# Kernel tuning notes

Measured on AMD Instinct MI355X. Metric: run time of the kernel, lower is better.

## Reference

```python
import jax, jax.numpy as jnp
import numpy as np

B, S, D, H = 1, 2048, 768, 12
E, K, I = 8, 2, 1024          # routed experts, top-k, expert inter dim
IS = 2 * I                    # shared-expert inter dim (n_shared_experts * moe_inter_dim)
EPS = 1e-5
ROUTE_SCALE = 1.0


def rmsnorm(x, w, eps=EPS):
    xf = x.astype(jnp.float32)
    return (xf * jax.lax.rsqrt(jnp.mean(xf * xf, axis=-1, keepdims=True) + eps)).astype(x.dtype) * w


def setup_inputs() -> dict:
    key = jax.random.key(0)
    ks = jax.random.split(key, 8)
    sc = 0.02
    return {
        "x": jax.random.normal(ks[0], (B, S, D), jnp.float32),
        "norm1_w": jnp.ones((D,), jnp.float32),
        "norm3_w": jnp.ones((D,), jnp.float32),
        "gate_w": jax.random.normal(ks[1], (E, D), jnp.float32) * sc,
        "w1": jax.random.normal(ks[2], (E, I, D), jnp.float32) * sc,
        "b1": jnp.zeros((E, I), jnp.float32),
        "w2": jax.random.normal(ks[3], (E, D, I), jnp.float32) * sc,
        "b2": jnp.zeros((E, D), jnp.float32),
        "w3": jax.random.normal(ks[4], (E, I, D), jnp.float32) * sc,
        "b3": jnp.zeros((E, I), jnp.float32),
        "fc1_w": jax.random.normal(ks[5], (IS, D), jnp.float32) * sc,
        "fc1_b": jnp.zeros((IS,), jnp.float32),
        "fc2_w": jax.random.normal(ks[6], (D, IS), jnp.float32) * sc,
        "fc2_b": jnp.zeros((D,), jnp.float32),
    }


def _forward(x, norm1_w, norm3_w, gate_w, w1, b1, w2, b2, w3, b3,
             fc1_w, fc1_b, fc2_w, fc2_b):
    b, s, d = x.shape
    hd = d // H

    # ---- self-attention (no qkv/out projections in the original module) ----
    xn = rmsnorm(x, norm1_w)
    qkv = xn.reshape(b, s, H, hd).transpose(0, 2, 1, 3)      # [b,h,s,hd]
    scores = jnp.einsum("bhqd,bhkd->bhqk", qkv, qkv) / np.sqrt(hd)
    attn = jax.nn.softmax(scores, axis=-1)
    ao = jnp.einsum("bhqk,bhkd->bhqd", attn, qkv)
    attn_out = ao.transpose(0, 2, 1, 3).reshape(b, s, d)
    out = x + attn_out

    # ---- MoE on norm3(out) ----
    xf = rmsnorm(out, norm3_w).reshape(-1, d)                # [N, D]
    n = xf.shape[0]

    # Gate: softmax scoring, n_groups=1 (no group masking), no bias (dim != 7168)
    logits = xf @ gate_w.T                                    # [N, E]
    sc = jax.nn.softmax(logits.astype(jnp.float32), axis=-1)  # max-subtract folded in
    _, idx = jax.lax.top_k(sc, K)                             # [N, K]
    weights = jnp.take_along_axis(sc, idx, axis=-1)
    weights = jnp.clip(weights, 1e-7) * ROUTE_SCALE
    weights = weights.astype(xf.dtype)

    # combine matrix: per-token dense expert weights (zeros for unselected)
    cmb = jnp.zeros((n, E), xf.dtype).at[jnp.arange(n)[:, None], idx].add(weights)

    # SwiGLU experts, batched over E (zero combine weight == not dispatched)
    a = jnp.einsum("nd,eid->nei", xf, w1) + b1                # [N,E,I]
    g = jnp.einsum("nd,eid->nei", xf, w3) + b3
    h = jax.nn.silu(a) * g
    eo = jnp.einsum("nei,edi->ned", h, w2) + b2               # [N,E,D]
    y = jnp.einsum("ned,ne->nd", eo, cmb)

    # shared experts (SiLU MLP)
    z = jax.nn.silu(xf @ fc1_w.T + fc1_b) @ fc2_w.T + fc2_b

    moe_out = (y + z).reshape(b, s, d)
    return out + moe_out


def reference(x, norm1_w, norm3_w, gate_w, w1, b1, w2, b2, w3, b3,
              fc1_w, fc1_b, fc2_w, fc2_b):
    return _forward(x, norm1_w, norm3_w, gate_w, w1, b1, w2, b2, w3, b3,
                    fc1_w, fc1_b, fc2_w, fc2_b)
```

## Files before the change

### kernel.cpp

```cpp
#include <hip/hip_runtime.h>
#include <math.h>

#define SEQ    2048
#define DMODEL 768
#define NHEAD  12
#define NEXP   8
#define IDIM   1024
#define ISH    2048
#define KVS    4
#define NE2    10

typedef unsigned short u16;
typedef short s16x8 __attribute__((ext_vector_type(8)));
typedef u16   u16x8 __attribute__((ext_vector_type(8)));
typedef float f32x4 __attribute__((ext_vector_type(4)));

#define MFMA_BF16(a, b, c) __builtin_amdgcn_mfma_f32_16x16x32_bf16((a), (b), (c), 0, 0, 0)

__device__ __forceinline__ void glds16(const void* g, void* l) {
  __builtin_amdgcn_global_load_lds(
      (const __attribute__((address_space(1))) unsigned int*)g,
      (__attribute__((address_space(3))) unsigned int*)l, 16, 0, 0);
}

__device__ __forceinline__ u16 f2b(float f) {
  unsigned int u = __float_as_uint(f);
  unsigned int r = u + 0x7fffu + ((u >> 16) & 1u);
  return (u16)(r >> 16);
}
__device__ __forceinline__ float b2f(u16 v) {
  return __uint_as_float(((unsigned int)v) << 16);
}

#define CVT_BLOCKS 10752

__global__ __launch_bounds__(256) void prep_kernel(
    const float* __restrict__ w1, const float* __restrict__ w3, const float* __restrict__ w2,
    const float* __restrict__ fc1, const float* __restrict__ fc2,
    u16* __restrict__ w1b, u16* __restrict__ w3b, u16* __restrict__ w2b,
    u16* __restrict__ fc1b, u16* __restrict__ fc2b, int* __restrict__ counts,
    const float* __restrict__ x, const float* __restrict__ norm1_w, u16* __restrict__ xnb) {
  __shared__ float red[256];
  const int tid = threadIdx.x;
  if (blockIdx.x < CVT_BLOCKS) {
    if (blockIdx.x == 0 && tid < 16) counts[tid] = 0;
    long i = (long)blockIdx.x * 256 + tid;
    const long NW8 = (long)NEXP * IDIM * DMODEL / 8;
    const long NF8 = (long)ISH * DMODEL / 8;
    const float* s; u16* d; long o;
    if      (i < NW8)             { s = w1;  d = w1b;  o = i; }
    else if (i < 2 * NW8)         { s = w3;  d = w3b;  o = i - NW8; }
    else if (i < 3 * NW8)         { s = w2;  d = w2b;  o = i - 2 * NW8; }
    else if (i < 3 * NW8 + NF8)   { s = fc1; d = fc1b; o = i - 3 * NW8; }
    else                          { s = fc2; d = fc2b; o = i - 3 * NW8 - NF8; }
    float4 a = ((const float4*)s)[2 * o], b = ((const float4*)s)[2 * o + 1];
    u16x8 v;
    v[0] = f2b(a.x); v[1] = f2b(a.y); v[2] = f2b(a.z); v[3] = f2b(a.w);
    v[4] = f2b(b.x); v[5] = f2b(b.y); v[6] = f2b(b.z); v[7] = f2b(b.w);
    ((u16x8*)d)[o] = v;
    return;
  }
  const int row = blockIdx.x - CVT_BLOCKS;
  const float* r = x + (size_t)row * DMODEL;
  float v0 = r[tid], v1 = r[tid + 256], v2 = r[tid + 512];
  float ss = v0 * v0 + v1 * v1 + v2 * v2;
  red[tid] = ss;
  __syncthreads();
  for (int s = 128; s > 0; s >>= 1) {
    if (tid < s) red[tid] += red[tid + s];
    __syncthreads();
  }
  float rms = rsqrtf(red[0] * (1.f / DMODEL) + 1e-5f);
  u16* ob = xnb + (size_t)row * DMODEL;
  ob[tid]       = f2b(v0 * rms * norm1_w[tid]);
  ob[tid + 256] = f2b(v1 * rms * norm1_w[tid + 256]);
  ob[tid + 512] = f2b(v2 * rms * norm1_w[tid + 512]);
}

__global__ __launch_bounds__(256) void attn_kernel(const u16* __restrict__ xnb,
                                                   u16* __restrict__ Opart,
                                                   float* __restrict__ Mpart,
                                                   float* __restrict__ Lpart) {
  __shared__ u16 Qs[64][72];
  __shared__ u16 Ks[64][72];
  __shared__ u16 Vt[64][72];
  __shared__ u16 Ps[64][72];
  const int h = blockIdx.y, kvs = blockIdx.z;
  const int q0 = blockIdx.x * 64;
  const int tid = threadIdx.x;
  const int lane = tid & 63, w = tid >> 6;
  const int quad = lane >> 4, l15 = lane & 15;
  const size_t hoff = (size_t)h * 64;

  for (int cc = tid; cc < 512; cc += 256) {
    int row = cc >> 3, col8 = (cc & 7) * 8;
    *(u16x8*)&Qs[row][col8] = *(const u16x8*)(xnb + (size_t)(q0 + row) * DMODEL + hoff + col8);
  }
  __syncthreads();
  const s16x8 aq0 = *(const s16x8*)&Qs[16 * w + l15][quad * 8];
  const s16x8 aq1 = *(const s16x8*)&Qs[16 * w + l15][32 + quad * 8];

  f32x4 o[4] = {};
  float mrow[4], lrow[4];
#pragma unroll
  for (int r = 0; r < 4; r++) { mrow[r] = -INFINITY; lrow[r] = 0.f; }

  const int it0 = kvs * (SEQ / 64 / KVS);
  for (int it = 0; it < SEQ / 64 / KVS; it++) {
    const int k0 = (it0 + it) * 64;
    for (int cc = tid; cc < 512; cc += 256) {
      int row = cc >> 3, col8 = (cc & 7) * 8;
      *(u16x8*)&Ks[row][col8] = *(const u16x8*)(xnb + (size_t)(k0 + row) * DMODEL + hoff + col8);
    }
    __syncthreads();

    {
      const int rp = tid & 31, dc = ((tid >> 5) & 7) * 8;
      u16x8 v0 = *(const u16x8*)&Ks[2 * rp][dc];
      u16x8 v1 = *(const u16x8*)&Ks[2 * rp + 1][dc];
#pragma unroll
      for (int j = 0; j < 8; j++) {
        *(unsigned int*)&Vt[dc + j][2 * rp] =
            (unsigned int)v0[j] | ((unsigned int)v1[j] << 16);
      }
    }

    f32x4 s4[4] = {};
#pragma unroll
    for (int jt = 0; jt < 4; jt++) {
      s16x8 b0 = *(const s16x8*)&Ks[16 * jt + l15][quad * 8];
      s16x8 b1 = *(const s16x8*)&Ks[16 * jt + l15][32 + quad * 8];
      s4[jt] = MFMA_BF16(aq0, b0, s4[jt]);
      s4[jt] = MFMA_BF16(aq1, b1, s4[jt]);
      s4[jt] *= 0.125f;
    }

#pragma unroll
    for (int r = 0; r < 4; r++) {
      float mx = mrow[r];
#pragma unroll
      for (int jt = 0; jt < 4; jt++) mx = fmaxf(mx, s4[jt][r]);
#pragma unroll
      for (int m = 1; m <= 8; m <<= 1) mx = fmaxf(mx, __shfl_xor(mx, m, 64));
      float al = __expf(mrow[r] - mx);
      mrow[r] = mx;
      float pv[4], sum = 0.f;
#pragma unroll
      for (int jt = 0; jt < 4; jt++) { pv[jt] = __expf(s4[jt][r] - mx); sum += pv[jt]; }
#pragma unroll
      for (int m = 1; m <= 8; m <<= 1) sum += __shfl_xor(sum, m, 64);
      lrow[r] = lrow[r] * al + sum;
#pragma unroll
      for (int jt = 0; jt < 4; jt++) o[jt][r] *= al;
#pragma unroll
      for (int jt = 0; jt < 4; jt++) Ps[16 * w + quad * 4 + r][16 * jt + l15] = f2b(pv[jt]);
    }
    __syncthreads();

    s16x8 ap0 = *(const s16x8*)&Ps[16 * w + l15][quad * 8];
    s16x8 ap1 = *(const s16x8*)&Ps[16 * w + l15][32 + quad * 8];
#pragma unroll
    for (int jt = 0; jt < 4; jt++) {
      s16x8 bv0 = *(const s16x8*)&Vt[16 * jt + l15][quad * 8];
      s16x8 bv1 = *(const s16x8*)&Vt[16 * jt + l15][32 + quad * 8];
      o[jt] = MFMA_BF16(ap0, bv0, o[jt]);
      o[jt] = MFMA_BF16(ap1, bv1, o[jt]);
    }
  }

  const size_t base = ((size_t)kvs * NHEAD + h) * SEQ;
#pragma unroll
  for (int r = 0; r < 4; r++) {
    int q = q0 + 16 * w + quad * 4 + r;
#pragma unroll
    for (int jt = 0; jt < 4; jt++)
      Opart[(base + q) * 64 + 16 * jt + l15] = f2b(o[jt][r]);
    if (l15 == 0) {
      Mpart[base + q] = mrow[r];
      Lpart[base + q] = lrow[r];
    }
  }
}

__global__ __launch_bounds__(256) void fused_post_kernel(
    const u16* __restrict__ Opart, const float* __restrict__ Mpart,
    const float* __restrict__ Lpart, const float* __restrict__ x,
    const float* __restrict__ n3w, const float* __restrict__ gw,
    u16* __restrict__ xfb, float* __restrict__ out,
    int* __restrict__ counts, int* __restrict__ toklist, float* __restrict__ wtlist) {
  const int t = blockIdx.x;
  const int tid = threadIdx.x;
  __shared__ float Ms[KVS * NHEAD], Ls[KVS * NHEAD];
  __shared__ float red[256];
  __shared__ float gred[4][NEXP];
  if (tid < KVS * NHEAD) {
    Ms[tid] = Mpart[(size_t)tid * SEQ + t];
    Ls[tid] = Lpart[(size_t)tid * SEQ + t];
  }
  __syncthreads();

  float val[3];
  float ss = 0.f;
#pragma unroll
  for (int ii = 0; ii < 3; ii++) {
    int c = tid + ii * 256;
    int h = c >> 6, d = c & 63;
    float M = -INFINITY;
#pragma unroll
    for (int k = 0; k < KVS; k++) M = fmaxf(M, Ms[k * NHEAD + h]);
    float L = 0.f, O = 0.f;
#pragma unroll
    for (int k = 0; k < KVS; k++) {
      float wgt = __expf(Ms[k * NHEAD + h] - M);
      L += wgt * Ls[k * NHEAD + h];
      O += wgt * b2f(Opart[((size_t)(k * NHEAD + h) * SEQ + t) * 64 + d]);
    }
    float v = x[(size_t)t * DMODEL + c] + O / L;
    out[(size_t)t * DMODEL + c] = v;
    val[ii] = v;
    ss += v * v;
  }
  red[tid] = ss;
  __syncthreads();
  for (int s = 128; s > 0; s >>= 1) {
    if (tid < s) red[tid] += red[tid + s];
    __syncthreads();
  }
  float rms = rsqrtf(red[0] * (1.f / DMODEL) + 1e-5f);

  float ge[NEXP] = {};
#pragma unroll
  for (int ii = 0; ii < 3; ii++) {
    int c = tid + ii * 256;
    float xn = val[ii] * rms * n3w[c];
    xfb[(size_t)t * DMODEL + c] = f2b(xn);
#pragma unroll
    for (int e = 0; e < NEXP; e++) ge[e] = fmaf(xn, gw[e * DMODEL + c], ge[e]);
  }
  const int lane = tid & 63, w = tid >> 6;
#pragma unroll
  for (int off = 32; off >= 1; off >>= 1)
#pragma unroll
    for (int e = 0; e < NEXP; e++) ge[e] += __shfl_xor(ge[e], off, 64);
  if (lane == 0)
#pragma unroll
    for (int e = 0; e < NEXP; e++) gred[w][e] = ge[e];
  __syncthreads();
  if (tid == 0) {
    float p[NEXP], mx = -INFINITY, s = 0.f;
#pragma unroll
    for (int e = 0; e < NEXP; e++) {
      p[e] = gred[0][e] + gred[1][e] + gred[2][e] + gred[3][e];
      mx = fmaxf(mx, p[e]);
    }
#pragma unroll
    for (int e = 0; e < NEXP; e++) { p[e] = __expf(p[e] - mx); s += p[e]; }
    int e0 = 0; float b0 = p[0];
    for (int e = 1; e < NEXP; e++) if (p[e] > b0) { b0 = p[e]; e0 = e; }
    int e1 = -1; float b1v = -1.f;
    for (int e = 0; e < NEXP; e++) if (e != e0 && p[e] > b1v) { b1v = p[e]; e1 = e; }
    float inv = 1.f / s;
    int pos0 = atomicAdd(&counts[e0], 1);
    toklist[e0 * SEQ + pos0] = t;
    wtlist[e0 * SEQ + pos0] = fmaxf(b0 * inv, 1e-7f);
    int pos1 = atomicAdd(&counts[e1], 1);
    toklist[e1 * SEQ + pos1] = t;
    wtlist[e1 * SEQ + pos1] = fmaxf(b1v * inv, 1e-7f);
  }
}

__global__ __launch_bounds__(256) void gemm1_kernel(
    const u16* __restrict__ xfb,
    const u16* __restrict__ w1b, const u16* __restrict__ w3b, const u16* __restrict__ fc1b,
    const float* __restrict__ b1, const float* __restrict__ b3, const float* __restrict__ fc1_b,
    const int* __restrict__ counts, const int* __restrict__ toklist, u16* __restrict__ hb) {
  __shared__ u16 As0[64][32],  As1[64][32];
  __shared__ u16 W1s0[128][32], W1s1[128][32];
  __shared__ u16 W3s0[128][32], W3s1[128][32];
  __shared__ int rIdx[64];
  const int L = blockIdx.x;
  const int g = L & 7, s = L >> 3;
  const int T = g * 320 + s;
  const int e = T >> 8;
  const int rem = T & 255;
  const int mt = rem >> 3, nt = rem & 7;
  const bool routed = (e < NEXP);
  int cnt, off;
  if (routed) {
    cnt = counts[e];
    off = 0;
    for (int i = 0; i < e; i++) off += counts[i];
  } else {
    cnt = SEQ;
    off = 2 * SEQ + (e - NEXP) * SEQ;
  }
  const int m0 = mt * 64;
  if (m0 >= cnt) return;
  const int n0 = nt * 128;
  const int tid = threadIdx.x;
  if (tid < 64) {
    int rr = m0 + tid;
    rIdx[tid] = routed ? toklist[e * SEQ + (rr < cnt ? rr : cnt - 1)] : rr;
  }
  __syncthreads();
  const u16* W1 = routed ? w1b + (size_t)e * IDIM * DMODEL
                         : fc1b + (size_t)(e - NEXP) * IDIM * DMODEL;
  const u16* W3 = w3b + (size_t)(routed ? e : 0) * IDIM * DMODEL;

  const int lane = tid & 63, w = tid >> 6;
  const int quad = lane >> 4, l15 = lane & 15;
  const int wy = w >> 1, wx = w & 1;
  const int rsub = lane >> 2, c8 = (lane & 3) * 8;
  const u16* Ap   = xfb + (size_t)rIdx[16 * w + rsub] * DMODEL + c8;
  const u16* W1p0 = W1 + (size_t)(n0 + 32 * w + rsub) * DMODEL + c8;
  const u16* W1p1 = W1 + (size_t)(n0 + 32 * w + 16 + rsub) * DMODEL + c8;
  const u16* W3p0 = W3 + (size_t)(n0 + 32 * w + rsub) * DMODEL + c8;
  const u16* W3p1 = W3 + (size_t)(n0 + 32 * w + 16 + rsub) * DMODEL + c8;

  f32x4 acc1[2][4] = {};
  f32x4 acc3[2][4] = {};
  for (int k0 = 0; k0 < DMODEL; k0 += 64) {
    glds16(Ap + k0,        &As0[16 * w][0]);
    glds16(Ap + k0 + 32,   &As1[16 * w][0]);
    glds16(W1p0 + k0,      &W1s0[32 * w][0]);
    glds16(W1p1 + k0,      &W1s0[32 * w + 16][0]);
    glds16(W1p0 + k0 + 32, &W1s1[32 * w][0]);
    glds16(W1p1 + k0 + 32, &W1s1[32 * w + 16][0]);
    if (routed) {
      glds16(W3p0 + k0,      &W3s0[32 * w][0]);
      glds16(W3p1 + k0,      &W3s0[32 * w + 16][0]);
      glds16(W3p0 + k0 + 32, &W3s1[32 * w][0]);
      glds16(W3p1 + k0 + 32, &W3s1[32 * w + 16][0]);
    }
    __syncthreads();
    s16x8 af0[2], af1[2], w1f0[4], w1f1[4];
#pragma unroll
    for (int i = 0; i < 2; i++) {
      af0[i] = *(const s16x8*)&As0[32 * wy + 16 * i + l15][quad * 8];
      af1[i] = *(const s16x8*)&As1[32 * wy + 16 * i + l15][quad * 8];
    }
#pragma unroll
    for (int j = 0; j < 4; j++) {
      w1f0[j] = *(const s16x8*)&W1s0[64 * wx + 16 * j + l15][quad * 8];
      w1f1[j] = *(const s16x8*)&W1s1[64 * wx + 16 * j + l15][quad * 8];
    }
#pragma unroll
    for (int i = 0; i < 2; i++)
#pragma unroll
      for (int j = 0; j < 4; j++) {
        acc1[i][j] = MFMA_BF16(af0[i], w1f0[j], acc1[i][j]);
        acc1[i][j] = MFMA_BF16(af1[i], w1f1[j], acc1[i][j]);
      }
    if (routed) {
      s16x8 w3f0[4], w3f1[4];
#pragma unroll
      for (int j = 0; j < 4; j++) {
        w3f0[j] = *(const s16x8*)&W3s0[64 * wx + 16 * j + l15][quad * 8];
        w3f1[j] = *(const s16x8*)&W3s1[64 * wx + 16 * j + l15][quad * 8];
      }
#pragma unroll
      for (int i = 0; i < 2; i++)
#pragma unroll
        for (int j = 0; j < 4; j++) {
          acc3[i][j] = MFMA_BF16(af0[i], w3f0[j], acc3[i][j]);
          acc3[i][j] = MFMA_BF16(af1[i], w3f1[j], acc3[i][j]);
        }
    }
    __syncthreads();
  }

#pragma unroll
  for (int j = 0; j < 4; j++) {
    int n = n0 + 64 * wx + 16 * j + l15;
    float b1v = routed ? b1[e * IDIM + n] : fc1_b[(e - NEXP) * IDIM + n];
    float b3v = routed ? b3[e * IDIM + n] : 0.f;
#pragma unroll
    for (int i = 0; i < 2; i++) {
#pragma unroll
      for (int r = 0; r < 4; r++) {
        int rr = m0 + 32 * wy + 16 * i + quad * 4 + r;
        if (rr < cnt) {
          float a = acc1[i][j][r] + b1v;
          float gg = routed ? (acc3[i][j][r] + b3v) : 1.f;
          float hv = a / (1.f + __expf(-a)) * gg;
          hb[(size_t)(off + rr) * IDIM + n] = f2b(hv);
        }
      }
    }
  }
}

__global__ __launch_bounds__(256) void gemm2_kernel(
    const u16* __restrict__ hb,
    const u16* __restrict__ w2b, const u16* __restrict__ fc2b,
    const float* __restrict__ b2, const float* __restrict__ fc2_b,
    const int* __restrict__ counts, const int* __restrict__ toklist,
    const float* __restrict__ wtlist, float* __restrict__ out) {
  __shared__ u16 As0[64][32],  As1[64][32];
  __shared__ u16 Ws0[128][32], Ws1[128][32];
  const int L = blockIdx.x;
  const int g = L & 7, s = L >> 3;
  const int T = g * 240 + s;
  const int e = T / 192;
  const int rem = T - e * 192;
  const int mt = rem / 6, nt = rem - mt * 6;
  const bool routed = (e < NEXP);
  int cnt, off;
  if (routed) {
    cnt = counts[e];
    off = 0;
    for (int i = 0; i < e; i++) off += counts[i];
  } else {
    cnt = SEQ;
    off = 2 * SEQ + (e - NEXP) * SEQ;
  }
  const int m0 = mt * 64;
  if (m0 >= cnt) return;
  const int n0 = nt * 128;
  const int tid = threadIdx.x;

  const u16* Wb; int ldw, kof;
  if (routed) { Wb = w2b + (size_t)e * DMODEL * IDIM; ldw = IDIM; kof = 0; }
  else        { Wb = fc2b;                            ldw = ISH;  kof = (e - NEXP) * IDIM; }

  const int lane = tid & 63, w = tid >> 6;
  const int quad = lane >> 4, l15 = lane & 15;
  const int wy = w >> 1, wx = w & 1;
  const int rsub = lane >> 2, c8 = (lane & 3) * 8;
  int ra = m0 + 16 * w + rsub; ra = off + (ra < cnt ? ra : cnt - 1);
  const u16* Ap  = hb + (size_t)ra * IDIM + c8;
  const u16* Wp0 = Wb + (size_t)(n0 + 32 * w + rsub) * ldw + kof + c8;
  const u16* Wp1 = Wb + (size_t)(n0 + 32 * w + 16 + rsub) * ldw + kof + c8;

  f32x4 acc[2][4] = {};
  for (int k0 = 0; k0 < IDIM; k0 += 64) {
    glds16(Ap + k0,        &As0[16 * w][0]);
    glds16(Ap + k0 + 32,   &As1[16 * w][0]);
    glds16(Wp0 + k0,       &Ws0[32 * w][0]);
    glds16(Wp1 + k0,       &Ws0[32 * w + 16][0]);
    glds16(Wp0 + k0 + 32,  &Ws1[32 * w][0]);
    glds16(Wp1 + k0 + 32,  &Ws1[32 * w + 16][0]);
    __syncthreads();
    s16x8 af0[2], af1[2], wf0[4], wf1[4];
#pragma unroll
    for (int i = 0; i < 2; i++) {
      af0[i] = *(const s16x8*)&As0[32 * wy + 16 * i + l15][quad * 8];
      af1[i] = *(const s16x8*)&As1[32 * wy + 16 * i + l15][quad * 8];
    }
#pragma unroll
    for (int j = 0; j < 4; j++) {
      wf0[j] = *(const s16x8*)&Ws0[64 * wx + 16 * j + l15][quad * 8];
      wf1[j] = *(const s16x8*)&Ws1[64 * wx + 16 * j + l15][quad * 8];
    }
#pragma unroll
    for (int i = 0; i < 2; i++)
#pragma unroll
      for (int j = 0; j < 4; j++) {
        acc[i][j] = MFMA_BF16(af0[i], wf0[j], acc[i][j]);
        acc[i][j] = MFMA_BF16(af1[i], wf1[j], acc[i][j]);
      }
    __syncthreads();
  }

#pragma unroll
  for (int j = 0; j < 4; j++) {
    int n = n0 + 64 * wx + 16 * j + l15;
    float bv = routed ? b2[e * DMODEL + n] : (e == NEXP ? fc2_b[n] : 0.f);
#pragma unroll
    for (int i = 0; i < 2; i++) {
#pragma unroll
      for (int r = 0; r < 4; r++) {
        int rr = m0 + 32 * wy + 16 * i + quad * 4 + r;
        if (rr < cnt) {
          int tok; float wt;
          if (routed) { tok = toklist[e * SEQ + rr]; wt = wtlist[e * SEQ + rr]; }
          else        { tok = rr;                    wt = 1.f; }
          atomicAdd(&out[(size_t)tok * DMODEL + n], wt * (acc[i][j][r] + bv));
        }
      }
    }
  }
}

extern "C" void kernel_launch(void* const* d_in, const int* in_sizes, int n_in,
                              void* d_out, int out_size, void* d_ws, size_t ws_size,
                              hipStream_t stream) {
  const float* x       = (const float*)d_in[0];
  const float* norm1_w = (const float*)d_in[1];
  const float* norm3_w = (const float*)d_in[2];
  const float* gate_w  = (const float*)d_in[3];
  const float* w1      = (const float*)d_in[4];
  const float* b1      = (const float*)d_in[5];
  const float* w2      = (const float*)d_in[6];
  const float* b2      = (const float*)d_in[7];
  const float* w3      = (const float*)d_in[8];
  const float* b3      = (const float*)d_in[9];
  const float* fc1_w   = (const float*)d_in[10];
  const float* fc1_b   = (const float*)d_in[11];
  const float* fc2_w   = (const float*)d_in[12];
  const float* fc2_b   = (const float*)d_in[13];
  float* out = (float*)d_out;

  char* p = (char*)d_ws;
  u16*   xnb    = (u16*)p;   p += (size_t)SEQ * DMODEL * 2;
  u16*   xfb    = (u16*)p;   p += (size_t)SEQ * DMODEL * 2;
  u16*   hb     = (u16*)p;   p += (size_t)4 * SEQ * IDIM * 2;
  u16*   Opart  = (u16*)p;   p += (size_t)KVS * NHEAD * SEQ * 64 * 2;
  float* Mpart  = (float*)p; p += (size_t)KVS * NHEAD * SEQ * 4;
  float* Lpart  = (float*)p; p += (size_t)KVS * NHEAD * SEQ * 4;
  u16*   w1b    = (u16*)p;   p += (size_t)NEXP * IDIM * DMODEL * 2;
  u16*   w3b    = (u16*)p;   p += (size_t)NEXP * IDIM * DMODEL * 2;
  u16*   w2b    = (u16*)p;   p += (size_t)NEXP * DMODEL * IDIM * 2;
  u16*   fc1b   = (u16*)p;   p += (size_t)ISH * DMODEL * 2;
  u16*   fc2b   = (u16*)p;   p += (size_t)DMODEL * ISH * 2;
  int*   counts = (int*)p;   p += 256;
  int*   toklist= (int*)p;   p += (size_t)NEXP * SEQ * 4;
  float* wtlist = (float*)p; p += (size_t)NEXP * SEQ * 4;

  prep_kernel<<<CVT_BLOCKS + SEQ, 256, 0, stream>>>(
      w1, w3, w2, fc1_w, fc2_w, w1b, w3b, w2b, fc1b, fc2b, counts, x, norm1_w, xnb);
  attn_kernel<<<dim3(SEQ / 64, NHEAD, KVS), 256, 0, stream>>>(xnb, Opart, Mpart, Lpart);
  fused_post_kernel<<<SEQ, 256, 0, stream>>>(Opart, Mpart, Lpart, x, norm3_w, gate_w,
                                             xfb, out, counts, toklist, wtlist);
  gemm1_kernel<<<2560, 256, 0, stream>>>(
      xfb, w1b, w3b, fc1b, b1, b3, fc1_b, counts, toklist, hb);
  gemm2_kernel<<<1920, 256, 0, stream>>>(
      hb, w2b, fc2b, b2, fc2_b, counts, toklist, wtlist, out);
  (void)in_sizes; (void)n_in; (void)out_size; (void)ws_size;
}
```

Before: 376.4 us.

## Stream expert weights directly to registers and double-buffer activation tiles in LDS

```diff
diff --git a/kernel.cpp b/kernel.cpp
--- a/kernel.cpp
+++ b/kernel.cpp
@@ -274,9 +274,7 @@
     const u16* __restrict__ w1b, const u16* __restrict__ w3b, const u16* __restrict__ fc1b,
     const float* __restrict__ b1, const float* __restrict__ b3, const float* __restrict__ fc1_b,
     const int* __restrict__ counts, const int* __restrict__ toklist, u16* __restrict__ hb) {
-  __shared__ u16 As0[64][32],  As1[64][32];
-  __shared__ u16 W1s0[128][32], W1s1[128][32];
-  __shared__ u16 W3s0[128][32], W3s1[128][32];
+  __shared__ u16 Abuf[2][2][64][32];
   __shared__ int rIdx[64];
   const int L = blockIdx.x;
   const int g = L & 7, s = L >> 3;
@@ -311,62 +309,51 @@
   const int quad = lane >> 4, l15 = lane & 15;
   const int wy = w >> 1, wx = w & 1;
   const int rsub = lane >> 2, c8 = (lane & 3) * 8;
-  const u16* Ap   = xfb + (size_t)rIdx[16 * w + rsub] * DMODEL + c8;
-  const u16* W1p0 = W1 + (size_t)(n0 + 32 * w + rsub) * DMODEL + c8;
-  const u16* W1p1 = W1 + (size_t)(n0 + 32 * w + 16 + rsub) * DMODEL + c8;
-  const u16* W3p0 = W3 + (size_t)(n0 + 32 * w + rsub) * DMODEL + c8;
-  const u16* W3p1 = W3 + (size_t)(n0 + 32 * w + 16 + rsub) * DMODEL + c8;
+  const u16* Ap  = xfb + (size_t)rIdx[16 * w + rsub] * DMODEL + c8;
+  const u16* W1r = W1 + (size_t)(n0 + 64 * wx + l15) * DMODEL + quad * 8;
+  const u16* W3r = W3 + (size_t)(n0 + 64 * wx + l15) * DMODEL + quad * 8;
 
   f32x4 acc1[2][4] = {};
   f32x4 acc3[2][4] = {};
-  for (int k0 = 0; k0 < DMODEL; k0 += 64) {
-    glds16(Ap + k0,        &As0[16 * w][0]);
-    glds16(Ap + k0 + 32,   &As1[16 * w][0]);
-    glds16(W1p0 + k0,      &W1s0[32 * w][0]);
-    glds16(W1p1 + k0,      &W1s0[32 * w + 16][0]);
-    glds16(W1p0 + k0 + 32, &W1s1[32 * w][0]);
-    glds16(W1p1 + k0 + 32, &W1s1[32 * w + 16][0]);
-    if (routed) {
-      glds16(W3p0 + k0,      &W3s0[32 * w][0]);
-      glds16(W3p1 + k0,      &W3s0[32 * w + 16][0]);
-      glds16(W3p0 + k0 + 32, &W3s1[32 * w][0]);
-      glds16(W3p1 + k0 + 32, &W3s1[32 * w + 16][0]);
-    }
+  const int NK = DMODEL / 64;
+
+  glds16(Ap, &Abuf[0][0][16 * w][0]);
+  glds16(Ap + 32, &Abuf[0][1][16 * w][0]);
+
+  for (int kt = 0; kt < NK; kt++) {
     __syncthreads();
-    s16x8 af0[2], af1[2], w1f0[4], w1f1[4];
-#pragma unroll
-    for (int i = 0; i < 2; i++) {
-      af0[i] = *(const s16x8*)&As0[32 * wy + 16 * i + l15][quad * 8];
-      af1[i] = *(const s16x8*)&As1[32 * wy + 16 * i + l15][quad * 8];
-    }
-#pragma unroll
-    for (int j = 0; j < 4; j++) {
-      w1f0[j] = *(const s16x8*)&W1s0[64 * wx + 16 * j + l15][quad * 8];
-      w1f1[j] = *(const s16x8*)&W1s1[64 * wx + 16 * j + l15][quad * 8];
-    }
-#pragma unroll
-    for (int i = 0; i < 2; i++)
-#pragma unroll
-      for (int j = 0; j < 4; j++) {
-        acc1[i][j] = MFMA_BF16(af0[i], w1f0[j], acc1[i][j]);
-        acc1[i][j] = MFMA_BF16(af1[i], w1f1[j], acc1[i][j]);
+    const int b = kt & 1;
+    if (kt + 1 < NK) {
+      glds16(Ap + (kt + 1) * 64, &Abuf[b ^ 1][0][16 * w][0]);
+      glds16(Ap + (kt + 1) * 64 + 32, &Abuf[b ^ 1][1][16 * w][0]);
+    }
+#pragma unroll
+    for (int p = 0; p < 2; p++) {
+      const int kc = kt * 64 + 32 * p;
+      s16x8 af[2];
+      af[0] = *(const s16x8*)&Abuf[b][p][32 * wy + l15][quad * 8];
+      af[1] = *(const s16x8*)&Abuf[b][p][32 * wy + 16 + l15][quad * 8];
+      s16x8 w1f[4];
+#pragma unroll
+      for (int j = 0; j < 4; j++)
+        w1f[j] = *(const s16x8*)(W1r + (size_t)(16 * j) * DMODEL + kc);
+#pragma unroll
+      for (int i = 0; i < 2; i++)
+#pragma unroll
+        for (int j = 0; j < 4; j++)
+          acc1[i][j] = MFMA_BF16(af[i], w1f[j], acc1[i][j]);
+      if (routed) {
+        s16x8 w3f[4];
+#pragma unroll
+        for (int j = 0; j < 4; j++)
+          w3f[j] = *(const s16x8*)(W3r + (size_t)(16 * j) * DMODEL + kc);
+#pragma unroll
+        for (int i = 0; i < 2; i++)
+#pragma unroll
+          for (int j = 0; j < 4; j++)
+            acc3[i][j] = MFMA_BF16(af[i], w3f[j], acc3[i][j]);
       }
-    if (routed) {
-      s16x8 w3f0[4], w3f1[4];
-#pragma unroll
-      for (int j = 0; j < 4; j++) {
-        w3f0[j] = *(const s16x8*)&W3s0[64 * wx + 16 * j + l15][quad * 8];
-        w3f1[j] = *(const s16x8*)&W3s1[64 * wx + 16 * j + l15][quad * 8];
-      }
-#pragma unroll
-      for (int i = 0; i < 2; i++)
-#pragma unroll
-        for (int j = 0; j < 4; j++) {
-          acc3[i][j] = MFMA_BF16(af0[i], w3f0[j], acc3[i][j]);
-          acc3[i][j] = MFMA_BF16(af1[i], w3f1[j], acc3[i][j]);
-        }
-    }
-    __syncthreads();
+    }
   }
 
 #pragma unroll
@@ -396,8 +383,7 @@
     const float* __restrict__ b2, const float* __restrict__ fc2_b,
     const int* __restrict__ counts, const int* __restrict__ toklist,
     const float* __restrict__ wtlist, float* __restrict__ out) {
-  __shared__ u16 As0[64][32],  As1[64][32];
-  __shared__ u16 Ws0[128][32], Ws1[128][32];
+  __shared__ u16 Abuf[2][2][64][32];
   const int L = blockIdx.x;
   const int g = L & 7, s = L >> 3;
   const int T = g * 240 + s;
@@ -428,38 +414,38 @@
   const int wy = w >> 1, wx = w & 1;
   const int rsub = lane >> 2, c8 = (lane & 3) * 8;
   int ra = m0 + 16 * w + rsub; ra = off + (ra < cnt ? ra : cnt - 1);
-  const u16* Ap  = hb + (size_t)ra * IDIM + c8;
-  const u16* Wp0 = Wb + (size_t)(n0 + 32 * w + rsub) * ldw + kof + c8;
-  const u16* Wp1 = Wb + (size_t)(n0 + 32 * w + 16 + rsub) * ldw + kof + c8;
+  const u16* Ap = hb + (size_t)ra * IDIM + c8;
+  const u16* Wr = Wb + (size_t)(n0 + 64 * wx + l15) * ldw + kof + quad * 8;
 
   f32x4 acc[2][4] = {};
-  for (int k0 = 0; k0 < IDIM; k0 += 64) {
-    glds16(Ap + k0,        &As0[16 * w][0]);
-    glds16(Ap + k0 + 32,   &As1[16 * w][0]);
-    glds16(Wp0 + k0,       &Ws0[32 * w][0]);
-    glds16(Wp1 + k0,       &Ws0[32 * w + 16][0]);
-    glds16(Wp0 + k0 + 32,  &Ws1[32 * w][0]);
-    glds16(Wp1 + k0 + 32,  &Ws1[32 * w + 16][0]);
+  const int NK = IDIM / 64;
+
+  glds16(Ap, &Abuf[0][0][16 * w][0]);
+  glds16(Ap + 32, &Abuf[0][1][16 * w][0]);
+
+  for (int kt = 0; kt < NK; kt++) {
     __syncthreads();
-    s16x8 af0[2], af1[2], wf0[4], wf1[4];
-#pragma unroll
-    for (int i = 0; i < 2; i++) {
-      af0[i] = *(const s16x8*)&As0[32 * wy + 16 * i + l15][quad * 8];
-      af1[i] = *(const s16x8*)&As1[32 * wy + 16 * i + l15][quad * 8];
-    }
-#pragma unroll
-    for (int j = 0; j < 4; j++) {
-      wf0[j] = *(const s16x8*)&Ws0[64 * wx + 16 * j + l15][quad * 8];
-      wf1[j] = *(const s16x8*)&Ws1[64 * wx + 16 * j + l15][quad * 8];
-    }
-#pragma unroll
-    for (int i = 0; i < 2; i++)
-#pragma unroll
-      for (int j = 0; j < 4; j++) {
-        acc[i][j] = MFMA_BF16(af0[i], wf0[j], acc[i][j]);
-        acc[i][j] = MFMA_BF16(af1[i], wf1[j], acc[i][j]);
-      }
-    __syncthreads();
+    const int b = kt & 1;
+    if (kt + 1 < NK) {
+      glds16(Ap + (kt + 1) * 64, &Abuf[b ^ 1][0][16 * w][0]);
+      glds16(Ap + (kt + 1) * 64 + 32, &Abuf[b ^ 1][1][16 * w][0]);
+    }
+#pragma unroll
+    for (int p = 0; p < 2; p++) {
+      const int kc = kt * 64 + 32 * p;
+      s16x8 af[2];
+      af[0] = *(const s16x8*)&Abuf[b][p][32 * wy + l15][quad * 8];
+      af[1] = *(const s16x8*)&Abuf[b][p][32 * wy + 16 + l15][quad * 8];
+      s16x8 wf[4];
+#pragma unroll
+      for (int j = 0; j < 4; j++)
+        wf[j] = *(const s16x8*)(Wr + (size_t)(16 * j) * ldw + kc);
+#pragma unroll
+      for (int i = 0; i < 2; i++)
+#pragma unroll
+        for (int j = 0; j < 4; j++)
+          acc[i][j] = MFMA_BF16(af[i], wf[j], acc[i][j]);
+    }
   }
 
 #pragma unroll
```

After: 527.8 us. 40.2% more time.
